# Kernel optimization log

Measured on AMD Instinct MI355X. Metric: run time of the kernel, lower is better.

## Reference

```python
import jax, jax.numpy as jnp
import numpy as np
import math

B, N, K, H = 2, 2048, 1024, 16
S = K // H  # head dim = 64


def apply_rope(t):
    # t: [b, h, N, s] -> rotary position embedding (rotate-half convention)
    s = t.shape[-1]
    pos = jnp.arange(t.shape[2], dtype=jnp.float32)
    inv_freq = 1.0 / (10000.0 ** (jnp.arange(0, s, 2, dtype=jnp.float32) / s))
    ang = pos[:, None] * inv_freq[None, :]               # [N, s/2]
    cos = jnp.concatenate([jnp.cos(ang), jnp.cos(ang)], axis=-1)  # [N, s]
    sin = jnp.concatenate([jnp.sin(ang), jnp.sin(ang)], axis=-1)
    t1, t2 = t[..., : s // 2], t[..., s // 2:]
    rot = jnp.concatenate([-t2, t1], axis=-1)
    return t * cos + rot * sin


def setup_inputs() -> dict:
    key = jax.random.key(0)
    ks = jax.random.split(key, 6)
    sc = 1.0 / math.sqrt(K)
    x = jax.random.normal(ks[0], (B, N, K), dtype=jnp.float32)
    Wq = jax.random.normal(ks[1], (K, K), dtype=jnp.float32) * sc
    Wk = jax.random.normal(ks[2], (K, K), dtype=jnp.float32) * sc
    Wv = jax.random.normal(ks[3], (K, K), dtype=jnp.float32) * sc
    Wu = jax.random.normal(ks[4], (K, K), dtype=jnp.float32) * sc
    bu = jax.random.normal(ks[5], (K,), dtype=jnp.float32) * 0.01
    mask = jnp.tril(jnp.ones((N, N), dtype=jnp.int32))  # causal
    return {"x": x, "Wq": Wq, "Wk": Wk, "Wv": Wv, "Wu": Wu, "bu": bu, "mask": mask}


def reference(x, Wq, Wk, Wv, Wu, bu, mask):
    b, n, k = x.shape
    h, s = H, S
    # torch Linear: y = x @ W.T
    def proj(W):
        return (x @ W.T).reshape(b, n, h, s).transpose(0, 2, 1, 3)  # [b,h,n,s]
    Q = apply_rope(proj(Wq))
    Kh = apply_rope(proj(Wk))
    V = proj(Wv)
    scores = jnp.einsum('bhqs,bhks->bhqk', Q, Kh) / math.sqrt(s)
    scores = jnp.where(mask[None, None, :, :] == 0, -jnp.inf, scores)
    attn = jax.nn.softmax(scores, axis=-1)
    out = jnp.einsum('bhqk,bhks->bhqs', attn, V)           # [b,h,n,s]
    out = out.transpose(0, 2, 1, 3).reshape(b, n, k)
    return out @ Wu.T + bu
```

## Files before the change

kernel.cpp:

```cpp
#include <hip/hip_runtime.h>
#include <hip/hip_bf16.h>

#define Bq 2
#define Nq 2048
#define Kq 1024
#define Hq 16
#define Sq 64
#define Mq (Bq * Nq)

typedef __attribute__((ext_vector_type(4))) float f32x4;
typedef __attribute__((ext_vector_type(8))) short bf16x8;

__device__ unsigned short g_xb[(size_t)Mq * Kq];
__device__ unsigned short g_Wqb[Kq * Kq];
__device__ unsigned short g_Wkb[Kq * Kq];
__device__ unsigned short g_Wvb[Kq * Kq];
__device__ unsigned short g_Wub[Kq * Kq];
__device__ unsigned short g_Qb[(size_t)Bq * Hq * Nq * Sq];
__device__ unsigned short g_Kb[(size_t)Bq * Hq * Nq * Sq];
__device__ unsigned short g_Vb[(size_t)Bq * Hq * Nq * Sq];
__device__ unsigned short g_Vt[(size_t)Bq * Hq * Sq * Nq];
__device__ unsigned short g_Ao[(size_t)Mq * Kq];

__device__ __forceinline__ unsigned short f2bf(float f) {
    union { float f; unsigned int i; } u; u.f = f;
    unsigned int r = u.i + 0x7FFF + ((u.i >> 16) & 1);
    return (unsigned short)(r >> 16);
}
__device__ __forceinline__ float bf2f(unsigned short u) {
    union { unsigned int i; float f; } v; v.i = ((unsigned int)u) << 16;
    return v.f;
}
__device__ __forceinline__ void async16(const unsigned short* g, unsigned short* l) {
    __builtin_amdgcn_global_load_lds(
        (const __attribute__((address_space(1))) void*)g,
        (__attribute__((address_space(3))) void*)l, 16, 0, 0);
}

__global__ __launch_bounds__(256) void convert_all_kernel(
    const float* __restrict__ x,  const float* __restrict__ wq,
    const float* __restrict__ wk, const float* __restrict__ wv,
    const float* __restrict__ wu)
{
    int i = blockIdx.x * 256 + threadIdx.x;
    const float* src; unsigned short* dst; int off;
    if (i < 1048576) { src = x; dst = g_xb; off = i; }
    else {
        int j = i - 1048576;
        int which = j >> 18;
        off = j & 262143;
        src = (which == 0) ? wq : (which == 1) ? wk : (which == 2) ? wv : wu;
        dst = (which == 0) ? g_Wqb : (which == 1) ? g_Wkb : (which == 2) ? g_Wvb : g_Wub;
    }
    float4 v = ((const float4*)src)[off];
    ushort4 o;
    o.x = f2bf(v.x); o.y = f2bf(v.y); o.z = f2bf(v.z); o.w = f2bf(v.w);
    ((ushort4*)dst)[off] = o;
}

__global__ __launch_bounds__(256) void qkv_gemm_kernel()
{
    __shared__ __align__(16) unsigned short As[2][128][64];
    __shared__ __align__(16) unsigned short Bs[2][128][64];

    const int n0 = blockIdx.x * 128;
    const int m0 = blockIdx.y * 128;
    const int which = n0 >> 10;
    const unsigned short* A  = g_xb;
    const unsigned short* Bm = (which == 0) ? g_Wqb : (which == 1) ? g_Wkb : g_Wvb;
    unsigned short* dst      = (which == 0) ? g_Qb : (which == 1) ? g_Kb : g_Vb;
    const int nb = n0 & 1023;

    const int tid = threadIdx.x;
    const int w = tid >> 6, l = tid & 63;
    const int lane16 = l & 15, quad = l >> 4;
    const int wm = (w >> 1) * 64, wn = (w & 1) * 64;

    const int sr = l >> 3;
    const int sc = ((l & 7) ^ sr) * 8;
    const int rsw = (lane16 & 7);

    f32x4 acc[4][4];
#pragma unroll
    for (int mi = 0; mi < 4; ++mi)
#pragma unroll
        for (int ni = 0; ni < 4; ++ni) acc[mi][ni] = (f32x4){0.f, 0.f, 0.f, 0.f};

#pragma unroll
    for (int c = 0; c < 4; ++c) {
        async16(A  + (size_t)(m0 + 32 * w + 8 * c + sr) * Kq + sc, &As[0][32 * w + 8 * c][0]);
        async16(Bm + (size_t)(nb + 32 * w + 8 * c + sr) * Kq + sc, &Bs[0][32 * w + 8 * c][0]);
    }
    __syncthreads();

    int cur = 0;
    for (int kt = 0; kt < Kq; kt += 64) {
        if (kt + 64 < Kq) {
            int nxt = cur ^ 1;
#pragma unroll
            for (int c = 0; c < 4; ++c) {
                async16(A  + (size_t)(m0 + 32 * w + 8 * c + sr) * Kq + kt + 64 + sc, &As[nxt][32 * w + 8 * c][0]);
                async16(Bm + (size_t)(nb + 32 * w + 8 * c + sr) * Kq + kt + 64 + sc, &Bs[nxt][32 * w + 8 * c][0]);
            }
        }
#pragma unroll
        for (int ks = 0; ks < 2; ++ks) {
            bf16x8 af[4], bfr[4];
#pragma unroll
            for (int mi = 0; mi < 4; ++mi)
                af[mi]  = *(const bf16x8*)&As[cur][wm + mi * 16 + lane16][((ks * 4 + quad) ^ rsw) * 8];
#pragma unroll
            for (int ni = 0; ni < 4; ++ni)
                bfr[ni] = *(const bf16x8*)&Bs[cur][wn + ni * 16 + lane16][((ks * 4 + quad) ^ rsw) * 8];
#pragma unroll
            for (int mi = 0; mi < 4; ++mi)
#pragma unroll
                for (int ni = 0; ni < 4; ++ni)
                    acc[mi][ni] = __builtin_amdgcn_mfma_f32_16x16x32_bf16(af[mi], bfr[ni], acc[mi][ni], 0, 0, 0);
        }
        __syncthreads();
        cur ^= 1;
    }

#pragma unroll
    for (int mi = 0; mi < 4; ++mi)
#pragma unroll
        for (int ni = 0; ni < 4; ++ni)
#pragma unroll
            for (int r = 0; r < 4; ++r) {
                int m = m0 + wm + mi * 16 + quad * 4 + r;
                int n = n0 + wn + ni * 16 + lane16;
                unsigned short v = f2bf(acc[mi][ni][r]);
                int b = m >> 11, nn = m & 2047;
                int o = n & 1023, h = o >> 6, s = o & 63;
                dst[(((size_t)b * Hq + h) * Nq + nn) * Sq + s] = v;
            }
}

__global__ __launch_bounds__(256) void rope_vtrans_kernel()
{
    __shared__ unsigned short T[64][72];

    if (blockIdx.y < 2) {
        unsigned short* buf = (blockIdx.y == 0) ? g_Qb : g_Kb;
        const int idx = blockIdx.x * 256 + threadIdx.x;
        const int i  = idx & 31;
        const int n  = (idx >> 5) & (Nq - 1);
        const int bh = idx >> 16;
        const size_t base = ((size_t)bh * Nq + n) * Sq + i;

        float t1 = bf2f(buf[base]);
        float t2 = bf2f(buf[base + 32]);
        float inv_freq = exp2f((float)i * -0.41524101f);
        float ang = (float)n * inv_freq;
        float sn = __sinf(ang), cs = __cosf(ang);
        buf[base]      = f2bf(t1 * cs - t2 * sn);
        buf[base + 32] = f2bf(t2 * cs + t1 * sn);
    } else {
        if (blockIdx.x >= 1024) return;
        const int n0 = (blockIdx.x & 31) * 64;
        const int bh = blockIdx.x >> 5;
        const unsigned short* src = g_Vb + (size_t)bh * Nq * Sq;
        unsigned short* dst       = g_Vt + (size_t)bh * Sq * Nq;
        const int tid = threadIdx.x;
        const int r = tid >> 3, c8 = (tid & 7) * 8;

        uint4 a0 = *(const uint4*)(src + (size_t)(n0 + r) * Sq + c8);
        uint4 a1 = *(const uint4*)(src + (size_t)(n0 + r + 32) * Sq + c8);
        *(uint4*)&T[r][c8] = a0;
        *(uint4*)&T[r + 32][c8] = a1;
        __syncthreads();

        union { ushort4 u4[2]; unsigned short u[8]; } p0, p1;
#pragma unroll
        for (int j = 0; j < 8; ++j) { p0.u[j] = T[c8 + j][r]; p1.u[j] = T[c8 + j][r + 32]; }
        *(uint4*)(dst + (size_t)r * Nq + n0 + c8)        = *(uint4*)&p0;
        *(uint4*)(dst + (size_t)(r + 32) * Nq + n0 + c8) = *(uint4*)&p1;
    }
}

__global__ __launch_bounds__(256) void attn_kernel()
{
    const int bh = blockIdx.x;
    const int qt = 31 - (int)blockIdx.y;
    const int q0 = qt * 64;
    const unsigned short* Qp = g_Qb + (size_t)bh * Nq * Sq;
    const unsigned short* Kp = g_Kb + (size_t)bh * Nq * Sq;
    const unsigned short* Vp = g_Vt + (size_t)bh * Sq * Nq;

    __shared__ __align__(16) unsigned short Ks[2][64][64];
    __shared__ __align__(16) unsigned short Vs[2][64][64];
    __shared__ __align__(16) unsigned short On[16][72];
    __shared__ __align__(16) unsigned short Ps[64][72];

    const int tid = threadIdx.x;
    const int w = tid >> 6, l = tid & 63;
    const int lane16 = l & 15, quad = l >> 4;
    const int sr = l >> 3;
    const int sc = ((l & 7) ^ sr) * 8;
    const int rsw = (lane16 & 7);

    for (int i = tid; i < 16 * 72; i += 256)
        ((unsigned short*)On)[i] = (i < 64) ? 0x3F80 : 0;

    bf16x8 aq0 = *(const bf16x8*)(Qp + (size_t)(q0 + 16 * w + lane16) * Sq + quad * 8);
    bf16x8 aq1 = *(const bf16x8*)(Qp + (size_t)(q0 + 16 * w + lane16) * Sq + quad * 8 + 32);

    f32x4 Oacc[4];
    f32x4 Oext = (f32x4){0.f, 0.f, 0.f, 0.f};
#pragma unroll
    for (int ds = 0; ds < 4; ++ds) Oacc[ds] = (f32x4){0.f, 0.f, 0.f, 0.f};

    const float C1 = 0.18033688f;
    const float C2 = 11.54156036f;

    async16(Kp + (size_t)(16 * w + sr) * Sq + sc,     &Ks[0][16 * w][0]);
    async16(Kp + (size_t)(16 * w + 8 + sr) * Sq + sc, &Ks[0][16 * w + 8][0]);
    async16(Vp + (size_t)(16 * w + sr) * Nq + sc,     &Vs[0][16 * w][0]);
    async16(Vp + (size_t)(16 * w + 8 + sr) * Nq + sc, &Vs[0][16 * w + 8][0]);
    __syncthreads();

    int cur = 0;
    for (int kb = 0; kb <= qt; ++kb) {
        if (kb < qt) {
            int kn = (kb + 1) * 64;
            int nb2 = cur ^ 1;
            async16(Kp + (size_t)(kn + 16 * w + sr) * Sq + sc,     &Ks[nb2][16 * w][0]);
            async16(Kp + (size_t)(kn + 16 * w + 8 + sr) * Sq + sc, &Ks[nb2][16 * w + 8][0]);
            async16(Vp + (size_t)(16 * w + sr) * Nq + kn + sc,     &Vs[nb2][16 * w][0]);
            async16(Vp + (size_t)(16 * w + 8 + sr) * Nq + kn + sc, &Vs[nb2][16 * w + 8][0]);
        }

        f32x4 S[4];
#pragma unroll
        for (int kc = 0; kc < 4; ++kc) S[kc] = (f32x4){0.f, 0.f, 0.f, 0.f};
#pragma unroll
        for (int kc = 0; kc < 4; ++kc) {
            const unsigned short* krow = &Ks[cur][kc * 16 + lane16][0];
            bf16x8 bk0 = *(const bf16x8*)&krow[(quad ^ rsw) * 8];
            bf16x8 bk1 = *(const bf16x8*)&krow[((4 + quad) ^ rsw) * 8];
            S[kc] = __builtin_amdgcn_mfma_f32_16x16x32_bf16(aq0, bk0, S[kc], 0, 0, 0);
            S[kc] = __builtin_amdgcn_mfma_f32_16x16x32_bf16(aq1, bk1, S[kc], 0, 0, 0);
        }

        const int qbase = q0 + 16 * w + quad * 4;
        if (kb == qt) {
#pragma unroll
            for (int kc = 0; kc < 4; ++kc) {
                int kpos = kb * 64 + kc * 16 + lane16;
#pragma unroll
                for (int r = 0; r < 4; ++r)
                    S[kc][r] = (kpos <= qbase + r) ? exp2f(fmaf(S[kc][r], C1, -C2)) : 0.0f;
            }
        } else {
#pragma unroll
            for (int kc = 0; kc < 4; ++kc)
#pragma unroll
                for (int r = 0; r < 4; ++r)
                    S[kc][r] = exp2f(fmaf(S[kc][r], C1, -C2));
        }

#pragma unroll
        for (int kc = 0; kc < 4; ++kc)
#pragma unroll
            for (int r = 0; r < 4; ++r)
                Ps[16 * w + quad * 4 + r][kc * 16 + lane16] =
                    (unsigned short)(__float_as_uint(S[kc][r]) >> 16);

#pragma unroll
        for (int kk = 0; kk < 2; ++kk) {
            bf16x8 pa = *(const bf16x8*)&Ps[16 * w + lane16][kk * 32 + quad * 8];
            bf16x8 be = *(const bf16x8*)&On[lane16][kk * 32 + quad * 8];
#pragma unroll
            for (int ds = 0; ds < 4; ++ds) {
                bf16x8 vb = *(const bf16x8*)&Vs[cur][ds * 16 + lane16][((kk * 4 + quad) ^ rsw) * 8];
                Oacc[ds] = __builtin_amdgcn_mfma_f32_16x16x32_bf16(pa, vb, Oacc[ds], 0, 0, 0);
            }
            Oext = __builtin_amdgcn_mfma_f32_16x16x32_bf16(pa, be, Oext, 0, 0, 0);
        }

        __syncthreads();
        cur ^= 1;
    }

    const int b = bh >> 4, h = bh & 15;
    float inv[4];
#pragma unroll
    for (int r = 0; r < 4; ++r) {
        float lr = __shfl(Oext[r], quad * 16, 64);
        inv[r] = 1.0f / lr;
    }
#pragma unroll
    for (int ds = 0; ds < 4; ++ds)
#pragma unroll
        for (int r = 0; r < 4; ++r) {
            int nn = q0 + 16 * w + quad * 4 + r;
            g_Ao[((size_t)b * Nq + nn) * Kq + h * Sq + ds * 16 + lane16] =
                f2bf(Oacc[ds][r] * inv[r]);
        }
}

__global__ __launch_bounds__(256) void out_gemm_kernel(
    const float* __restrict__ bu, float* __restrict__ out)
{
    __shared__ __align__(16) unsigned short As[2][128][64];
    __shared__ __align__(16) unsigned short Bs[2][128][64];

    const int n0 = blockIdx.x * 128;
    const int m0 = blockIdx.y * 128;

    const int tid = threadIdx.x;
    const int w = tid >> 6, l = tid & 63;
    const int lane16 = l & 15, quad = l >> 4;
    const int wm = (w >> 1) * 64, wn = (w & 1) * 64;
    const int sr = l >> 3;
    const int sc = ((l & 7) ^ sr) * 8;
    const int rsw = (lane16 & 7);

    f32x4 acc[4][4];
#pragma unroll
    for (int mi = 0; mi < 4; ++mi)
#pragma unroll
        for (int ni = 0; ni < 4; ++ni) acc[mi][ni] = (f32x4){0.f, 0.f, 0.f, 0.f};

#pragma unroll
    for (int c = 0; c < 4; ++c) {
        async16(g_Ao  + (size_t)(m0 + 32 * w + 8 * c + sr) * Kq + sc, &As[0][32 * w + 8 * c][0]);
        async16(g_Wub + (size_t)(n0 + 32 * w + 8 * c + sr) * Kq + sc, &Bs[0][32 * w + 8 * c][0]);
    }
    __syncthreads();

    int cur = 0;
    for (int kt = 0; kt < Kq; kt += 64) {
        if (kt + 64 < Kq) {
            int nxt = cur ^ 1;
#pragma unroll
            for (int c = 0; c < 4; ++c) {
                async16(g_Ao  + (size_t)(m0 + 32 * w + 8 * c + sr) * Kq + kt + 64 + sc, &As[nxt][32 * w + 8 * c][0]);
                async16(g_Wub + (size_t)(n0 + 32 * w + 8 * c + sr) * Kq + kt + 64 + sc, &Bs[nxt][32 * w + 8 * c][0]);
            }
        }
#pragma unroll
        for (int ks = 0; ks < 2; ++ks) {
            bf16x8 af[4], bfr[4];
#pragma unroll
            for (int mi = 0; mi < 4; ++mi)
                af[mi]  = *(const bf16x8*)&As[cur][wm + mi * 16 + lane16][((ks * 4 + quad) ^ rsw) * 8];
#pragma unroll
            for (int ni = 0; ni < 4; ++ni)
                bfr[ni] = *(const bf16x8*)&Bs[cur][wn + ni * 16 + lane16][((ks * 4 + quad) ^ rsw) * 8];
#pragma unroll
            for (int mi = 0; mi < 4; ++mi)
#pragma unroll
                for (int ni = 0; ni < 4; ++ni)
                    acc[mi][ni] = __builtin_amdgcn_mfma_f32_16x16x32_bf16(af[mi], bfr[ni], acc[mi][ni], 0, 0, 0);
        }
        __syncthreads();
        cur ^= 1;
    }

#pragma unroll
    for (int mi = 0; mi < 4; ++mi)
#pragma unroll
        for (int ni = 0; ni < 4; ++ni)
#pragma unroll
            for (int r = 0; r < 4; ++r) {
                int m = m0 + wm + mi * 16 + quad * 4 + r;
                int n = n0 + wn + ni * 16 + lane16;
                out[(size_t)m * Kq + n] = acc[mi][ni][r] + bu[n];
            }
}

extern "C" void kernel_launch(void* const* d_in, const int* in_sizes, int n_in,
                              void* d_out, int out_size, void* d_ws, size_t ws_size,
                              hipStream_t stream)
{
    const float* x  = (const float*)d_in[0];
    const float* Wq = (const float*)d_in[1];
    const float* Wk = (const float*)d_in[2];
    const float* Wv = (const float*)d_in[3];
    const float* Wu = (const float*)d_in[4];
    const float* bu = (const float*)d_in[5];
    float* out = (float*)d_out;

    convert_all_kernel<<<8192, 256, 0, stream>>>(x, Wq, Wk, Wv, Wu);
    qkv_gemm_kernel<<<dim3(24, 32), 256, 0, stream>>>();
    rope_vtrans_kernel<<<dim3(8192, 3), 256, 0, stream>>>();
    attn_kernel<<<dim3(32, 32), 256, 0, stream>>>();
    out_gemm_kernel<<<dim3(8, 32), 256, 0, stream>>>(bu, out);
}
```

Before: 216.8 us.

## Fuse all stages into one persistent kernel with software grid barriers

Replaces the five launches (convert, QKV GEMM, RoPE/V-transpose, attention, output GEMM) with a single persistent kernel of 512 blocks. The stages are separated by a software grid barrier built on atomics in global memory. Attention work is paired per block, a late query tile with an early one, to balance the causal load. This removes launch gaps and tail effects. In exchange, 768 QKV tiles now run on 512 blocks (1.5 waves), the output GEMM uses only 256 blocks, and the barrier spin-waits. Correctness depends on all 512 blocks being co-resident, at 2 blocks per CU with 64KB shared memory each.

```diff
diff --git a/kernel.cpp b/kernel.cpp
--- a/kernel.cpp
+++ b/kernel.cpp
@@ -7,6 +7,7 @@
 #define Hq 16
 #define Sq 64
 #define Mq (Bq * Nq)
+#define NB 512
 
 typedef __attribute__((ext_vector_type(4))) float f32x4;
 typedef __attribute__((ext_vector_type(8))) short bf16x8;
@@ -22,6 +23,9 @@
 __device__ unsigned short g_Vt[(size_t)Bq * Hq * Sq * Nq];
 __device__ unsigned short g_Ao[(size_t)Mq * Kq];
 
+__device__ unsigned g_count = 0;
+__device__ unsigned g_gen   = 0;
+
 __device__ __forceinline__ unsigned short f2bf(float f) {
     union { float f; unsigned int i; } u; u.f = f;
     unsigned int r = u.i + 0x7FFF + ((u.i >> 16) & 1);
@@ -37,168 +41,37 @@
         (__attribute__((address_space(3))) void*)l, 16, 0, 0);
 }
 
-__global__ __launch_bounds__(256) void convert_all_kernel(
-    const float* __restrict__ x,  const float* __restrict__ wq,
-    const float* __restrict__ wk, const float* __restrict__ wv,
-    const float* __restrict__ wu)
+__device__ __forceinline__ void gbar() {
+    __syncthreads();
+    if (threadIdx.x == 0) {
+        __threadfence();
+        unsigned my = __hip_atomic_load(&g_gen, __ATOMIC_RELAXED, __HIP_MEMORY_SCOPE_AGENT);
+        unsigned old = __hip_atomic_fetch_add(&g_count, 1, __ATOMIC_ACQ_REL, __HIP_MEMORY_SCOPE_AGENT);
+        if (old == NB - 1) {
+            __hip_atomic_store(&g_count, 0, __ATOMIC_RELAXED, __HIP_MEMORY_SCOPE_AGENT);
+            __hip_atomic_fetch_add(&g_gen, 1, __ATOMIC_ACQ_REL, __HIP_MEMORY_SCOPE_AGENT);
+        } else {
+            while (__hip_atomic_load(&g_gen, __ATOMIC_ACQUIRE, __HIP_MEMORY_SCOPE_AGENT) == my)
+                __builtin_amdgcn_s_sleep(2);
+        }
+        __threadfence();
+    }
+    __syncthreads();
+}
+
+__device__ __forceinline__ void attn_one(int bh, int qt, unsigned char* smem,
+                                         int w, int lane16, int quad,
+                                         int sr, int sc, int rsw)
 {
-    int i = blockIdx.x * 256 + threadIdx.x;
-    const float* src; unsigned short* dst; int off;
-    if (i < 1048576) { src = x; dst = g_xb; off = i; }
-    else {
-        int j = i - 1048576;
-        int which = j >> 18;
-        off = j & 262143;
-        src = (which == 0) ? wq : (which == 1) ? wk : (which == 2) ? wv : wu;
-        dst = (which == 0) ? g_Wqb : (which == 1) ? g_Wkb : (which == 2) ? g_Wvb : g_Wub;
-    }
-    float4 v = ((const float4*)src)[off];
-    ushort4 o;
-    o.x = f2bf(v.x); o.y = f2bf(v.y); o.z = f2bf(v.z); o.w = f2bf(v.w);
-    ((ushort4*)dst)[off] = o;
-}
-
-__global__ __launch_bounds__(256) void qkv_gemm_kernel()
-{
-    __shared__ __align__(16) unsigned short As[2][128][64];
-    __shared__ __align__(16) unsigned short Bs[2][128][64];
-
-    const int n0 = blockIdx.x * 128;
-    const int m0 = blockIdx.y * 128;
-    const int which = n0 >> 10;
-    const unsigned short* A  = g_xb;
-    const unsigned short* Bm = (which == 0) ? g_Wqb : (which == 1) ? g_Wkb : g_Wvb;
-    unsigned short* dst      = (which == 0) ? g_Qb : (which == 1) ? g_Kb : g_Vb;
-    const int nb = n0 & 1023;
-
+    auto Ks = (unsigned short (*)[64][64])(smem);
+    auto Vs = (unsigned short (*)[64][64])(smem + 16384);
+    auto On = (unsigned short (*)[72])(smem + 32768);
+    auto Ps = (unsigned short (*)[72])(smem + 35072);
     const int tid = threadIdx.x;
-    const int w = tid >> 6, l = tid & 63;
-    const int lane16 = l & 15, quad = l >> 4;
-    const int wm = (w >> 1) * 64, wn = (w & 1) * 64;
-
-    const int sr = l >> 3;
-    const int sc = ((l & 7) ^ sr) * 8;
-    const int rsw = (lane16 & 7);
-
-    f32x4 acc[4][4];
-#pragma unroll
-    for (int mi = 0; mi < 4; ++mi)
-#pragma unroll
-        for (int ni = 0; ni < 4; ++ni) acc[mi][ni] = (f32x4){0.f, 0.f, 0.f, 0.f};
-
-#pragma unroll
-    for (int c = 0; c < 4; ++c) {
-        async16(A  + (size_t)(m0 + 32 * w + 8 * c + sr) * Kq + sc, &As[0][32 * w + 8 * c][0]);
-        async16(Bm + (size_t)(nb + 32 * w + 8 * c + sr) * Kq + sc, &Bs[0][32 * w + 8 * c][0]);
-    }
-    __syncthreads();
-
-    int cur = 0;
-    for (int kt = 0; kt < Kq; kt += 64) {
-        if (kt + 64 < Kq) {
-            int nxt = cur ^ 1;
-#pragma unroll
-            for (int c = 0; c < 4; ++c) {
-                async16(A  + (size_t)(m0 + 32 * w + 8 * c + sr) * Kq + kt + 64 + sc, &As[nxt][32 * w + 8 * c][0]);
-                async16(Bm + (size_t)(nb + 32 * w + 8 * c + sr) * Kq + kt + 64 + sc, &Bs[nxt][32 * w + 8 * c][0]);
-            }
-        }
-#pragma unroll
-        for (int ks = 0; ks < 2; ++ks) {
-            bf16x8 af[4], bfr[4];
-#pragma unroll
-            for (int mi = 0; mi < 4; ++mi)
-                af[mi]  = *(const bf16x8*)&As[cur][wm + mi * 16 + lane16][((ks * 4 + quad) ^ rsw) * 8];
-#pragma unroll
-            for (int ni = 0; ni < 4; ++ni)
-                bfr[ni] = *(const bf16x8*)&Bs[cur][wn + ni * 16 + lane16][((ks * 4 + quad) ^ rsw) * 8];
-#pragma unroll
-            for (int mi = 0; mi < 4; ++mi)
-#pragma unroll
-                for (int ni = 0; ni < 4; ++ni)
-                    acc[mi][ni] = __builtin_amdgcn_mfma_f32_16x16x32_bf16(af[mi], bfr[ni], acc[mi][ni], 0, 0, 0);
-        }
-        __syncthreads();
-        cur ^= 1;
-    }
-
-#pragma unroll
-    for (int mi = 0; mi < 4; ++mi)
-#pragma unroll
-        for (int ni = 0; ni < 4; ++ni)
-#pragma unroll
-            for (int r = 0; r < 4; ++r) {
-                int m = m0 + wm + mi * 16 + quad * 4 + r;
-                int n = n0 + wn + ni * 16 + lane16;
-                unsigned short v = f2bf(acc[mi][ni][r]);
-                int b = m >> 11, nn = m & 2047;
-                int o = n & 1023, h = o >> 6, s = o & 63;
-                dst[(((size_t)b * Hq + h) * Nq + nn) * Sq + s] = v;
-            }
-}
-
-__global__ __launch_bounds__(256) void rope_vtrans_kernel()
-{
-    __shared__ unsigned short T[64][72];
-
-    if (blockIdx.y < 2) {
-        unsigned short* buf = (blockIdx.y == 0) ? g_Qb : g_Kb;
-        const int idx = blockIdx.x * 256 + threadIdx.x;
-        const int i  = idx & 31;
-        const int n  = (idx >> 5) & (Nq - 1);
-        const int bh = idx >> 16;
-        const size_t base = ((size_t)bh * Nq + n) * Sq + i;
-
-        float t1 = bf2f(buf[base]);
-        float t2 = bf2f(buf[base + 32]);
-        float inv_freq = exp2f((float)i * -0.41524101f);
-        float ang = (float)n * inv_freq;
-        float sn = __sinf(ang), cs = __cosf(ang);
-        buf[base]      = f2bf(t1 * cs - t2 * sn);
-        buf[base + 32] = f2bf(t2 * cs + t1 * sn);
-    } else {
-        if (blockIdx.x >= 1024) return;
-        const int n0 = (blockIdx.x & 31) * 64;
-        const int bh = blockIdx.x >> 5;
-        const unsigned short* src = g_Vb + (size_t)bh * Nq * Sq;
-        unsigned short* dst       = g_Vt + (size_t)bh * Sq * Nq;
-        const int tid = threadIdx.x;
-        const int r = tid >> 3, c8 = (tid & 7) * 8;
-
-        uint4 a0 = *(const uint4*)(src + (size_t)(n0 + r) * Sq + c8);
-        uint4 a1 = *(const uint4*)(src + (size_t)(n0 + r + 32) * Sq + c8);
-        *(uint4*)&T[r][c8] = a0;
-        *(uint4*)&T[r + 32][c8] = a1;
-        __syncthreads();
-
-        union { ushort4 u4[2]; unsigned short u[8]; } p0, p1;
-#pragma unroll
-        for (int j = 0; j < 8; ++j) { p0.u[j] = T[c8 + j][r]; p1.u[j] = T[c8 + j][r + 32]; }
-        *(uint4*)(dst + (size_t)r * Nq + n0 + c8)        = *(uint4*)&p0;
-        *(uint4*)(dst + (size_t)(r + 32) * Nq + n0 + c8) = *(uint4*)&p1;
-    }
-}
-
-__global__ __launch_bounds__(256) void attn_kernel()
-{
-    const int bh = blockIdx.x;
-    const int qt = 31 - (int)blockIdx.y;
     const int q0 = qt * 64;
     const unsigned short* Qp = g_Qb + (size_t)bh * Nq * Sq;
     const unsigned short* Kp = g_Kb + (size_t)bh * Nq * Sq;
     const unsigned short* Vp = g_Vt + (size_t)bh * Sq * Nq;
-
-    __shared__ __align__(16) unsigned short Ks[2][64][64];
-    __shared__ __align__(16) unsigned short Vs[2][64][64];
-    __shared__ __align__(16) unsigned short On[16][72];
-    __shared__ __align__(16) unsigned short Ps[64][72];
-
-    const int tid = threadIdx.x;
-    const int w = tid >> 6, l = tid & 63;
-    const int lane16 = l & 15, quad = l >> 4;
-    const int sr = l >> 3;
-    const int sc = ((l & 7) ^ sr) * 8;
-    const int rsw = (lane16 & 7);
 
     for (int i = tid; i < 16 * 72; i += 256)
         ((unsigned short*)On)[i] = (i < 64) ? 0x3F80 : 0;
@@ -284,10 +157,11 @@
     }
 
     const int b = bh >> 4, h = bh & 15;
+    const int ll = threadIdx.x & 63;
     float inv[4];
 #pragma unroll
     for (int r = 0; r < 4; ++r) {
-        float lr = __shfl(Oext[r], quad * 16, 64);
+        float lr = __shfl(Oext[r], (ll >> 4) * 16, 64);
         inv[r] = 1.0f / lr;
     }
 #pragma unroll
@@ -300,75 +174,216 @@
         }
 }
 
-__global__ __launch_bounds__(256) void out_gemm_kernel(
-    const float* __restrict__ bu, float* __restrict__ out)
+__global__ __launch_bounds__(256, 2) void mega_kernel(
+    const float* __restrict__ x,  const float* __restrict__ wq,
+    const float* __restrict__ wk, const float* __restrict__ wv,
+    const float* __restrict__ wu, const float* __restrict__ bu,
+    float* __restrict__ out)
 {
-    __shared__ __align__(16) unsigned short As[2][128][64];
-    __shared__ __align__(16) unsigned short Bs[2][128][64];
-
-    const int n0 = blockIdx.x * 128;
-    const int m0 = blockIdx.y * 128;
-
+    __shared__ __align__(16) unsigned char smem[65536];
+
+    const int bid = blockIdx.x;
     const int tid = threadIdx.x;
     const int w = tid >> 6, l = tid & 63;
     const int lane16 = l & 15, quad = l >> 4;
     const int wm = (w >> 1) * 64, wn = (w & 1) * 64;
     const int sr = l >> 3;
     const int sc = ((l & 7) ^ sr) * 8;
-    const int rsw = (lane16 & 7);
-
-    f32x4 acc[4][4];
-#pragma unroll
-    for (int mi = 0; mi < 4; ++mi)
-#pragma unroll
-        for (int ni = 0; ni < 4; ++ni) acc[mi][ni] = (f32x4){0.f, 0.f, 0.f, 0.f};
-
-#pragma unroll
-    for (int c = 0; c < 4; ++c) {
-        async16(g_Ao  + (size_t)(m0 + 32 * w + 8 * c + sr) * Kq + sc, &As[0][32 * w + 8 * c][0]);
-        async16(g_Wub + (size_t)(n0 + 32 * w + 8 * c + sr) * Kq + sc, &Bs[0][32 * w + 8 * c][0]);
-    }
-    __syncthreads();
-
-    int cur = 0;
-    for (int kt = 0; kt < Kq; kt += 64) {
-        if (kt + 64 < Kq) {
-            int nxt = cur ^ 1;
+    const int rsw = lane16 & 7;
+
+    for (int i = bid * 256 + tid; i < 2097152; i += NB * 256) {
+        const float* src; unsigned short* dst; int off;
+        if (i < 1048576) { src = x; dst = g_xb; off = i; }
+        else {
+            int j = i - 1048576;
+            int which = j >> 18;
+            off = j & 262143;
+            src = (which == 0) ? wq : (which == 1) ? wk : (which == 2) ? wv : wu;
+            dst = (which == 0) ? g_Wqb : (which == 1) ? g_Wkb : (which == 2) ? g_Wvb : g_Wub;
+        }
+        float4 v = ((const float4*)src)[off];
+        ushort4 o;
+        o.x = f2bf(v.x); o.y = f2bf(v.y); o.z = f2bf(v.z); o.w = f2bf(v.w);
+        ((ushort4*)dst)[off] = o;
+    }
+    gbar();
+
+    {
+        auto As = (unsigned short (*)[128][64])(smem);
+        auto Bs = (unsigned short (*)[128][64])(smem + 32768);
+        for (int t = bid; t < 768; t += NB) {
+            const int nt = t % 24, mt = t / 24;
+            const int n0 = nt * 128, m0 = mt * 128;
+            const int which = n0 >> 10;
+            const unsigned short* A  = g_xb;
+            const unsigned short* Bm = (which == 0) ? g_Wqb : (which == 1) ? g_Wkb : g_Wvb;
+            unsigned short* dst      = (which == 0) ? g_Qb : (which == 1) ? g_Kb : g_Vb;
+            const int nb = n0 & 1023;
+
+            f32x4 acc[4][4];
+#pragma unroll
+            for (int mi = 0; mi < 4; ++mi)
+#pragma unroll
+                for (int ni = 0; ni < 4; ++ni) acc[mi][ni] = (f32x4){0.f, 0.f, 0.f, 0.f};
+
 #pragma unroll
             for (int c = 0; c < 4; ++c) {
-                async16(g_Ao  + (size_t)(m0 + 32 * w + 8 * c + sr) * Kq + kt + 64 + sc, &As[nxt][32 * w + 8 * c][0]);
-                async16(g_Wub + (size_t)(n0 + 32 * w + 8 * c + sr) * Kq + kt + 64 + sc, &Bs[nxt][32 * w + 8 * c][0]);
-            }
-        }
-#pragma unroll
-        for (int ks = 0; ks < 2; ++ks) {
-            bf16x8 af[4], bfr[4];
+                async16(A  + (size_t)(m0 + 32 * w + 8 * c + sr) * Kq + sc, &As[0][32 * w + 8 * c][0]);
+                async16(Bm + (size_t)(nb + 32 * w + 8 * c + sr) * Kq + sc, &Bs[0][32 * w + 8 * c][0]);
+            }
+            __syncthreads();
+
+            int cur = 0;
+            for (int kt = 0; kt < Kq; kt += 64) {
+                if (kt + 64 < Kq) {
+                    int nxt = cur ^ 1;
+#pragma unroll
+                    for (int c = 0; c < 4; ++c) {
+                        async16(A  + (size_t)(m0 + 32 * w + 8 * c + sr) * Kq + kt + 64 + sc, &As[nxt][32 * w + 8 * c][0]);
+                        async16(Bm + (size_t)(nb + 32 * w + 8 * c + sr) * Kq + kt + 64 + sc, &Bs[nxt][32 * w + 8 * c][0]);
+                    }
+                }
+#pragma unroll
+                for (int ks = 0; ks < 2; ++ks) {
+                    bf16x8 af[4], bfr[4];
+#pragma unroll
+                    for (int mi = 0; mi < 4; ++mi)
+                        af[mi]  = *(const bf16x8*)&As[cur][wm + mi * 16 + lane16][((ks * 4 + quad) ^ rsw) * 8];
+#pragma unroll
+                    for (int ni = 0; ni < 4; ++ni)
+                        bfr[ni] = *(const bf16x8*)&Bs[cur][wn + ni * 16 + lane16][((ks * 4 + quad) ^ rsw) * 8];
+#pragma unroll
+                    for (int mi = 0; mi < 4; ++mi)
+#pragma unroll
+                        for (int ni = 0; ni < 4; ++ni)
+                            acc[mi][ni] = __builtin_amdgcn_mfma_f32_16x16x32_bf16(af[mi], bfr[ni], acc[mi][ni], 0, 0, 0);
+                }
+                __syncthreads();
+                cur ^= 1;
+            }
+
 #pragma unroll
             for (int mi = 0; mi < 4; ++mi)
-                af[mi]  = *(const bf16x8*)&As[cur][wm + mi * 16 + lane16][((ks * 4 + quad) ^ rsw) * 8];
+#pragma unroll
+                for (int ni = 0; ni < 4; ++ni)
+#pragma unroll
+                    for (int r = 0; r < 4; ++r) {
+                        int m = m0 + wm + mi * 16 + quad * 4 + r;
+                        int n = n0 + wn + ni * 16 + lane16;
+                        unsigned short v = f2bf(acc[mi][ni][r]);
+                        int b = m >> 11, nn = m & 2047;
+                        int o = n & 1023, h = o >> 6, s = o & 63;
+                        dst[(((size_t)b * Hq + h) * Nq + nn) * Sq + s] = v;
+                    }
+        }
+    }
+    gbar();
+
+    for (int i = bid * 256 + tid; i < 2 * 2097152; i += NB * 256) {
+        unsigned short* buf = (i < 2097152) ? g_Qb : g_Kb;
+        const int idx = i & 2097151;
+        const int ii = idx & 31;
+        const int n  = (idx >> 5) & (Nq - 1);
+        const int bh = idx >> 16;
+        const size_t base = ((size_t)bh * Nq + n) * Sq + ii;
+        float t1 = bf2f(buf[base]);
+        float t2 = bf2f(buf[base + 32]);
+        float inv_freq = exp2f((float)ii * -0.41524101f);
+        float ang = (float)n * inv_freq;
+        float sn = __sinf(ang), cs = __cosf(ang);
+        buf[base]      = f2bf(t1 * cs - t2 * sn);
+        buf[base + 32] = f2bf(t2 * cs + t1 * sn);
+    }
+    {
+        auto T = (unsigned short (*)[72])(smem);
+        const int r = tid >> 3, c8 = (tid & 7) * 8;
+        for (int t = bid; t < 1024; t += NB) {
+            const int n0 = (t & 31) * 64;
+            const int bh = t >> 5;
+            const unsigned short* src = g_Vb + (size_t)bh * Nq * Sq;
+            unsigned short* dst       = g_Vt + (size_t)bh * Sq * Nq;
+            __syncthreads();
+            uint4 a0 = *(const uint4*)(src + (size_t)(n0 + r) * Sq + c8);
+            uint4 a1 = *(const uint4*)(src + (size_t)(n0 + r + 32) * Sq + c8);
+            *(uint4*)&T[r][c8] = a0;
+            *(uint4*)&T[r + 32][c8] = a1;
+            __syncthreads();
+            union { ushort4 u4[2]; unsigned short u[8]; } p0, p1;
+#pragma unroll
+            for (int j = 0; j < 8; ++j) { p0.u[j] = T[c8 + j][r]; p1.u[j] = T[c8 + j][r + 32]; }
+            *(uint4*)(dst + (size_t)r * Nq + n0 + c8)        = *(uint4*)&p0;
+            *(uint4*)(dst + (size_t)(r + 32) * Nq + n0 + c8) = *(uint4*)&p1;
+        }
+    }
+    gbar();
+
+    {
+        const int bh = bid & 31;
+        const int j  = bid >> 5;
+        attn_one(bh, 31 - j, smem, w, lane16, quad, sr, sc, rsw);
+        attn_one(bh, j,      smem, w, lane16, quad, sr, sc, rsw);
+    }
+    gbar();
+
+    if (bid < 256) {
+        auto As = (unsigned short (*)[128][64])(smem);
+        auto Bs = (unsigned short (*)[128][64])(smem + 32768);
+        const int n0 = (bid & 7) * 128;
+        const int m0 = (bid >> 3) * 128;
+
+        f32x4 acc[4][4];
+#pragma unroll
+        for (int mi = 0; mi < 4; ++mi)
+#pragma unroll
+            for (int ni = 0; ni < 4; ++ni) acc[mi][ni] = (f32x4){0.f, 0.f, 0.f, 0.f};
+
+#pragma unroll
+        for (int c = 0; c < 4; ++c) {
+            async16(g_Ao  + (size_t)(m0 + 32 * w + 8 * c + sr) * Kq + sc, &As[0][32 * w + 8 * c][0]);
+            async16(g_Wub + (size_t)(n0 + 32 * w + 8 * c + sr) * Kq + sc, &Bs[0][32 * w + 8 * c][0]);
+        }
+        __syncthreads();
+
+        int cur = 0;
+        for (int kt = 0; kt < Kq; kt += 64) {
+            if (kt + 64 < Kq) {
+                int nxt = cur ^ 1;
+#pragma unroll
+                for (int c = 0; c < 4; ++c) {
+                    async16(g_Ao  + (size_t)(m0 + 32 * w + 8 * c + sr) * Kq + kt + 64 + sc, &As[nxt][32 * w + 8 * c][0]);
+                    async16(g_Wub + (size_t)(n0 + 32 * w + 8 * c + sr) * Kq + kt + 64 + sc, &Bs[nxt][32 * w + 8 * c][0]);
+                }
+            }
+#pragma unroll
+            for (int ks = 0; ks < 2; ++ks) {
+                bf16x8 af[4], bfr[4];
+#pragma unroll
+                for (int mi = 0; mi < 4; ++mi)
+                    af[mi]  = *(const bf16x8*)&As[cur][wm + mi * 16 + lane16][((ks * 4 + quad) ^ rsw) * 8];
+#pragma unroll
+                for (int ni = 0; ni < 4; ++ni)
+                    bfr[ni] = *(const bf16x8*)&Bs[cur][wn + ni * 16 + lane16][((ks * 4 + quad) ^ rsw) * 8];
+#pragma unroll
+                for (int mi = 0; mi < 4; ++mi)
+#pragma unroll
+                    for (int ni = 0; ni < 4; ++ni)
+                        acc[mi][ni] = __builtin_amdgcn_mfma_f32_16x16x32_bf16(af[mi], bfr[ni], acc[mi][ni], 0, 0, 0);
+            }
+            __syncthreads();
+            cur ^= 1;
+        }
+
+#pragma unroll
+        for (int mi = 0; mi < 4; ++mi)
 #pragma unroll
             for (int ni = 0; ni < 4; ++ni)
-                bfr[ni] = *(const bf16x8*)&Bs[cur][wn + ni * 16 + lane16][((ks * 4 + quad) ^ rsw) * 8];
-#pragma unroll
-            for (int mi = 0; mi < 4; ++mi)
-#pragma unroll
-                for (int ni = 0; ni < 4; ++ni)
-                    acc[mi][ni] = __builtin_amdgcn_mfma_f32_16x16x32_bf16(af[mi], bfr[ni], acc[mi][ni], 0, 0, 0);
-        }
-        __syncthreads();
-        cur ^= 1;
-    }
-
-#pragma unroll
-    for (int mi = 0; mi < 4; ++mi)
-#pragma unroll
-        for (int ni = 0; ni < 4; ++ni)
-#pragma unroll
-            for (int r = 0; r < 4; ++r) {
-                int m = m0 + wm + mi * 16 + quad * 4 + r;
-                int n = n0 + wn + ni * 16 + lane16;
-                out[(size_t)m * Kq + n] = acc[mi][ni][r] + bu[n];
-            }
+#pragma unroll
+                for (int r = 0; r < 4; ++r) {
+                    int m = m0 + wm + mi * 16 + quad * 4 + r;
+                    int n = n0 + wn + ni * 16 + lane16;
+                    out[(size_t)m * Kq + n] = acc[mi][ni][r] + bu[n];
+                }
+    }
 }
 
 extern "C" void kernel_launch(void* const* d_in, const int* in_sizes, int n_in,
@@ -383,9 +398,5 @@
     const float* bu = (const float*)d_in[5];
     float* out = (float*)d_out;
 
-    convert_all_kernel<<<8192, 256, 0, stream>>>(x, Wq, Wk, Wv, Wu);
-    qkv_gemm_kernel<<<dim3(24, 32), 256, 0, stream>>>();
-    rope_vtrans_kernel<<<dim3(8192, 3), 256, 0, stream>>>();
-    attn_kernel<<<dim3(32, 32), 256, 0, stream>>>();
-    out_gemm_kernel<<<dim3(8, 32), 256, 0, stream>>>(bu, out);
-}
+    mega_kernel<<<NB, 256, 0, stream>>>(x, Wq, Wk, Wv, Wu, bu, out);
+}
```

After: 633.5 us. +192.2%, slower.
